# Kernel tuning notes

Measured on AMD Instinct MI355X. Metric: run time of the kernel, lower is better.

Reference implementation:

```python
import jax, jax.numpy as jnp
import numpy as np

B, N, E, DIN, H1, H2, DOUT = 2, 20000, 320000, 128, 256, 256, 128


def setup_inputs() -> dict:
    key = jax.random.key(0)
    ks = jax.random.split(key, 9)
    X = jax.random.normal(ks[0], (B, N, DIN), dtype=jnp.float32)
    edge_index = jax.random.randint(ks[1], (2, E), 0, N, dtype=jnp.int32)
    def lin(k, fan_in, fan_out):
        lim = 1.0 / np.sqrt(fan_in)
        return jax.random.uniform(k, (fan_in, fan_out), jnp.float32, -lim, lim)
    W1 = lin(ks[2], DIN, H1); b1 = jnp.zeros((H1,), jnp.float32)
    W2 = lin(ks[3], H1, H2);  b2 = jnp.zeros((H2,), jnp.float32)
    W3 = lin(ks[4], H2, DOUT); b3 = jnp.zeros((DOUT,), jnp.float32)
    prelu_a = jnp.array(0.25, jnp.float32)  # PReLU default single shared param
    return dict(X=X, W1=W1, b1=b1, W2=W2, b2=b2, W3=W3, b3=b3,
                prelu_a=prelu_a, edge_index=edge_index)


def reference(X, W1, b1, W2, b2, W3, b3, prelu_a, edge_index):
    src, dst = edge_index[0], edge_index[1]
    n = X.shape[1]
    # GCN symmetric normalization with self-loops: deg = in-degree + 1
    deg = jax.ops.segment_sum(jnp.ones_like(src, X.dtype), dst, num_segments=n) + 1.0
    dinv = jax.lax.rsqrt(deg)                      # [N]
    norm_e = dinv[src] * dinv[dst]                 # [E] edge norm
    norm_self = dinv * dinv                        # [N] self-loop norm

    def gcn(x, W, b):
        h = x @ W                                  # [N, F_out]
        agg = jax.ops.segment_sum(h[src] * norm_e[:, None], dst, num_segments=n)
        agg = agg + h * norm_self[:, None]         # add self-loop message
        return agg + b

    def prelu(x):
        return jnp.where(x >= 0, x, prelu_a * x)

    def single(x):  # x: [N, DIN]
        x = prelu(gcn(x, W1, b1))
        x = prelu(gcn(x, W2, b2))
        return gcn(x, W3, b3)

    return jax.vmap(single)(X)                     # [B, N, DOUT]
```

## Files before the change

kernel.cpp:

```cpp
#include <hip/hip_runtime.h>

#define NB 20000
#define EB 320000
#define DIN 128
#define H1D 256
#define H2D 256
#define DOUTD 128
#define SCAN_BLOCKS ((NB + 255) / 256)


__global__ void zero_kernel(int* __restrict__ p, int n) {
    int t = blockIdx.x * blockDim.x + threadIdx.x;
    if (t < n) p[t] = 0;
}

__global__ void hist_kernel(const int* __restrict__ dst, int* __restrict__ bins) {
    int t = blockIdx.x * blockDim.x + threadIdx.x;
    if (t < EB) atomicAdd(&bins[dst[t]], 1);
}

__global__ __launch_bounds__(256) void scanA_kernel(const int* __restrict__ bins,
                                                    int* __restrict__ loc,
                                                    int* __restrict__ blksum) {
    __shared__ int s[256];
    int t = threadIdx.x;
    int i = blockIdx.x * 256 + t;
    int v = (i < NB) ? bins[i] : 0;
    s[t] = v;
    __syncthreads();
    for (int off = 1; off < 256; off <<= 1) {
        int u = (t >= off) ? s[t - off] : 0;
        __syncthreads();
        s[t] += u;
        __syncthreads();
    }
    if (i < NB) loc[i] = s[t] - v;
    if (t == 255) blksum[blockIdx.x] = s[255];
}

__global__ __launch_bounds__(128) void scanB_kernel(int* __restrict__ blksum) {
    __shared__ int s[128];
    int t = threadIdx.x;
    int v = (t < SCAN_BLOCKS) ? blksum[t] : 0;
    s[t] = v;
    __syncthreads();
    for (int off = 1; off < 128; off <<= 1) {
        int u = (t >= off) ? s[t - off] : 0;
        __syncthreads();
        s[t] += u;
        __syncthreads();
    }
    if (t < SCAN_BLOCKS) blksum[t] = s[t] - v;
}

__global__ __launch_bounds__(256) void scanC_kernel(const int* __restrict__ bins,
                                                    const int* __restrict__ loc,
                                                    const int* __restrict__ blksum,
                                                    int* __restrict__ rs,
                                                    int* __restrict__ cursor,
                                                    float* __restrict__ dinv) {
    int i = blockIdx.x * 256 + threadIdx.x;
    if (i < NB) {
        int r = loc[i] + blksum[blockIdx.x];
        rs[i] = r;
        cursor[i] = r;
        dinv[i] = rsqrtf((float)bins[i] + 1.0f);
    }
    if (i == 0) rs[NB] = EB;
}

__global__ void scatter_kernel(const int* __restrict__ src, const int* __restrict__ dst,
                               const float* __restrict__ dinv,
                               int* __restrict__ cursor, int2* __restrict__ edges) {
    int t = blockIdx.x * blockDim.x + threadIdx.x;
    if (t < EB) {
        int d = dst[t], s = src[t];
        int p = atomicAdd(&cursor[d], 1);
        edges[p] = make_int2(s, __float_as_int(dinv[s] * dinv[d]));
    }
}


template <int NC>
__device__ inline void ldrow(float4 (&d)[NC], const float* __restrict__ p) {
#pragma unroll
    for (int c = 0; c < NC; ++c) d[c] = ((const float4*)p)[c];
}
template <int NC>
__device__ inline void fmarow(float4 (&a)[NC], const float4 (&t)[NC], float w) {
#pragma unroll
    for (int c = 0; c < NC; ++c) {
        a[c].x = fmaf(t[c].x, w, a[c].x);
        a[c].y = fmaf(t[c].y, w, a[c].y);
        a[c].z = fmaf(t[c].z, w, a[c].z);
        a[c].w = fmaf(t[c].w, w, a[c].w);
    }
}

template <int F, bool SPLIT_IN, bool SPLIT_OUT, bool BIAS, bool PRELU>
__global__ __launch_bounds__(256) void agg_kernel(
    const float* __restrict__ h, float* __restrict__ out,
    const int* __restrict__ rs, const int2* __restrict__ edges,
    const float* __restrict__ dinv, const float* __restrict__ bias,
    const float* __restrict__ pa) {
    constexpr int V2 = 2 * F / 64;
    constexpr int NC = V2 / 4;
    constexpr int GSTRIDE = SPLIT_IN ? F : 2 * F;
    int node = blockIdx.x * 4 + (threadIdx.x >> 6);
    int lane = threadIdx.x & 63;
    int b = lane >> 5;
    int fl = (lane & 31) * V2;

    const float* gbase = SPLIT_IN ? (h + (size_t)b * NB * F + fl)
                                  : (h + (size_t)lane * V2);

    float4 acc0[NC], acc1[NC], acc2[NC], acc3[NC];
    {
        float dv = dinv[node];
        float sw = dv * dv;
        float4 tv[NC];
        ldrow<NC>(tv, gbase + (size_t)node * GSTRIDE);
#pragma unroll
        for (int c = 0; c < NC; ++c) {
            acc0[c] = make_float4(tv[c].x * sw, tv[c].y * sw, tv[c].z * sw, tv[c].w * sw);
            acc1[c] = make_float4(0.f, 0.f, 0.f, 0.f);
            acc2[c] = make_float4(0.f, 0.f, 0.f, 0.f);
            acc3[c] = make_float4(0.f, 0.f, 0.f, 0.f);
        }
    }

    int e0 = __builtin_amdgcn_readfirstlane(rs[node]);
    int e1 = __builtin_amdgcn_readfirstlane(rs[node + 1]);
    int e = e0;
    for (; e + 4 <= e1; e += 4) {
        int2 d0 = edges[e], d1 = edges[e + 1], d2 = edges[e + 2], d3 = edges[e + 3];
        float4 t0[NC], t1[NC], t2[NC], t3[NC];
        ldrow<NC>(t0, gbase + (size_t)d0.x * GSTRIDE);
        ldrow<NC>(t1, gbase + (size_t)d1.x * GSTRIDE);
        ldrow<NC>(t2, gbase + (size_t)d2.x * GSTRIDE);
        ldrow<NC>(t3, gbase + (size_t)d3.x * GSTRIDE);
        fmarow<NC>(acc0, t0, __int_as_float(d0.y));
        fmarow<NC>(acc1, t1, __int_as_float(d1.y));
        fmarow<NC>(acc2, t2, __int_as_float(d2.y));
        fmarow<NC>(acc3, t3, __int_as_float(d3.y));
    }
    for (; e < e1; ++e) {
        int2 d0 = edges[e];
        float4 t0[NC];
        ldrow<NC>(t0, gbase + (size_t)d0.x * GSTRIDE);
        fmarow<NC>(acc0, t0, __int_as_float(d0.y));
    }

#pragma unroll
    for (int c = 0; c < NC; ++c) {
        acc0[c].x += (acc1[c].x + acc2[c].x) + acc3[c].x;
        acc0[c].y += (acc1[c].y + acc2[c].y) + acc3[c].y;
        acc0[c].z += (acc1[c].z + acc2[c].z) + acc3[c].z;
        acc0[c].w += (acc1[c].w + acc2[c].w) + acc3[c].w;
    }
    if (BIAS) {
        float4 bv[NC];
        ldrow<NC>(bv, bias + fl);
#pragma unroll
        for (int c = 0; c < NC; ++c) {
            acc0[c].x += bv[c].x; acc0[c].y += bv[c].y;
            acc0[c].z += bv[c].z; acc0[c].w += bv[c].w;
        }
    }
    if (PRELU) {
        float a = *pa;
#pragma unroll
        for (int c = 0; c < NC; ++c) {
            acc0[c].x = acc0[c].x >= 0.f ? acc0[c].x : a * acc0[c].x;
            acc0[c].y = acc0[c].y >= 0.f ? acc0[c].y : a * acc0[c].y;
            acc0[c].z = acc0[c].z >= 0.f ? acc0[c].z : a * acc0[c].z;
            acc0[c].w = acc0[c].w >= 0.f ? acc0[c].w : a * acc0[c].w;
        }
    }
    float* obase = SPLIT_OUT ? (out + (size_t)b * NB * F + (size_t)node * F + fl)
                             : (out + (size_t)node * 2 * F + lane * V2);
#pragma unroll
    for (int c = 0; c < NC; ++c) ((float4*)obase)[c] = acc0[c];
}

template <bool BIAS, bool PRELU>
__global__ __launch_bounds__(256) void gemm_kernel(const float* __restrict__ A, int M, int K,
                                                   const float* __restrict__ W, int Nc,
                                                   const float* __restrict__ bias,
                                                   const float* __restrict__ pa,
                                                   float* __restrict__ C) {
    __shared__ alignas(16) float As[16][132];
    __shared__ alignas(16) float Bs[16][68];
    int t = threadIdx.x;
    int bm = blockIdx.x * 128;
    int bn = blockIdx.y * 64;
    int tx = t & 15, ty = t >> 4;
    int m0 = ty * 8, n0 = tx * 4;
    int ar = t >> 2, ac4 = (t & 3) * 4;
    int br = t >> 4, bc4 = (t & 15) * 4;

    float acc[8][4] = {};

    for (int k0 = 0; k0 < K; k0 += 16) {
        float4 a0 = make_float4(0.f, 0.f, 0.f, 0.f), a1 = a0;
        int r0 = bm + ar, r1 = bm + ar + 64;
        if (r0 < M) a0 = *(const float4*)&A[(size_t)r0 * K + k0 + ac4];
        if (r1 < M) a1 = *(const float4*)&A[(size_t)r1 * K + k0 + ac4];
        As[ac4 + 0][ar] = a0.x; As[ac4 + 1][ar] = a0.y;
        As[ac4 + 2][ar] = a0.z; As[ac4 + 3][ar] = a0.w;
        As[ac4 + 0][ar + 64] = a1.x; As[ac4 + 1][ar + 64] = a1.y;
        As[ac4 + 2][ar + 64] = a1.z; As[ac4 + 3][ar + 64] = a1.w;
        float4 bv = *(const float4*)&W[(size_t)(k0 + br) * Nc + bn + bc4];
        *(float4*)&Bs[br][bc4] = bv;
        __syncthreads();
#pragma unroll
        for (int k = 0; k < 16; ++k) {
            float4 av0 = *(const float4*)&As[k][m0];
            float4 av1 = *(const float4*)&As[k][m0 + 4];
            float4 bv4 = *(const float4*)&Bs[k][n0];
            float a_[8] = {av0.x, av0.y, av0.z, av0.w, av1.x, av1.y, av1.z, av1.w};
            float b_[4] = {bv4.x, bv4.y, bv4.z, bv4.w};
#pragma unroll
            for (int i = 0; i < 8; ++i)
#pragma unroll
                for (int j = 0; j < 4; ++j)
                    acc[i][j] = fmaf(a_[i], b_[j], acc[i][j]);
        }
        __syncthreads();
    }

    float pav = 0.0f;
    if (PRELU) pav = *pa;
#pragma unroll
    for (int i = 0; i < 8; ++i) {
        int row = bm + m0 + i;
        if (row < M) {
            float v[4];
#pragma unroll
            for (int j = 0; j < 4; ++j) {
                float x = acc[i][j];
                if (BIAS) x += bias[bn + n0 + j];
                if (PRELU) x = (x >= 0.0f) ? x : pav * x;
                v[j] = x;
            }
            *(float4*)&C[(size_t)row * Nc + bn + n0] = make_float4(v[0], v[1], v[2], v[3]);
        }
    }
}


static inline char* carve(char*& p, size_t bytes) {
    char* r = p;
    p += (bytes + 255) & ~(size_t)255;
    return r;
}

extern "C" void kernel_launch(void* const* d_in, const int* in_sizes, int n_in,
                              void* d_out, int out_size, void* d_ws, size_t ws_size,
                              hipStream_t stream) {
    const float* X  = (const float*)d_in[0];
    const float* W1 = (const float*)d_in[1];
    const float* b1 = (const float*)d_in[2];
    const float* W2 = (const float*)d_in[3];
    const float* b2 = (const float*)d_in[4];
    const float* W3 = (const float*)d_in[5];
    const float* b3 = (const float*)d_in[6];
    const float* pa = (const float*)d_in[7];
    const int* ei   = (const int*)d_in[8];
    const int* src = ei;
    const int* dst = ei + EB;
    float* out = (float*)d_out;

    char* p = (char*)d_ws;
    int* bins    = (int*)carve(p, NB * sizeof(int));
    int* loc     = (int*)carve(p, NB * sizeof(int));
    int* blksum  = (int*)carve(p, 128 * sizeof(int));
    int* rs      = (int*)carve(p, (NB + 1) * sizeof(int));
    int* cursor  = (int*)carve(p, NB * sizeof(int));
    int2* edges  = (int2*)carve(p, EB * sizeof(int2));
    float* dinv  = (float*)carve(p, NB * sizeof(float));
    float* bufA  = (float*)carve(p, (size_t)2 * NB * 256 * sizeof(float));
    float* bufB  = (float*)carve(p, (size_t)2 * NB * 256 * sizeof(float));

    const int M = 2 * NB;

    zero_kernel<<<SCAN_BLOCKS, 256, 0, stream>>>(bins, NB);
    hist_kernel<<<(EB + 255) / 256, 256, 0, stream>>>(dst, bins);
    scanA_kernel<<<SCAN_BLOCKS, 256, 0, stream>>>(bins, loc, blksum);
    scanB_kernel<<<1, 128, 0, stream>>>(blksum);
    scanC_kernel<<<SCAN_BLOCKS, 256, 0, stream>>>(bins, loc, blksum, rs, cursor, dinv);
    scatter_kernel<<<(EB + 255) / 256, 256, 0, stream>>>(src, dst, dinv, cursor, edges);

    const int aggGrid = NB / 4;

    agg_kernel<128, true, false, false, false><<<aggGrid, 256, 0, stream>>>(
        X, bufA, rs, edges, dinv, nullptr, nullptr);
    gemm_kernel<true, true><<<dim3((M + 127) / 128, H1D / 64), 256, 0, stream>>>(
        bufA, M, DIN, W1, H1D, b1, pa, bufB);

    gemm_kernel<false, false><<<dim3((M + 127) / 128, H2D / 64), 256, 0, stream>>>(
        bufB, M, H1D, W2, H2D, nullptr, nullptr, bufA);
    agg_kernel<256, false, false, true, true><<<aggGrid, 256, 0, stream>>>(
        bufA, bufB, rs, edges, dinv, b2, pa);

    gemm_kernel<false, false><<<dim3((M + 127) / 128, DOUTD / 64), 256, 0, stream>>>(
        bufB, M, H2D, W3, DOUTD, nullptr, nullptr, bufA);
    agg_kernel<128, false, true, true, false><<<aggGrid, 256, 0, stream>>>(
        bufA, out, rs, edges, dinv, b3, nullptr);
}
```

Measured before the change: 394.9 us.

## Slice aggregation features into eight column slabs so gathers stay cache-resident

Replaces the one-node-per-wavefront aggregation kernel with a sliced version. Each block handles one of eight feature slices for a chunk of 160 nodes, and several nodes share a wavefront with a few lanes each. Restricting each block to an F/8 column slab shrinks the working set of the random neighbour gathers, which should raise L2/MALL hit rates. Edge records are read with nontemporal loads. In exchange, the edge list and row pointers are re-read eight times, each lane holds fewer accumulators and gets less memory-level parallelism per edge, and lanes diverge because neighbouring nodes in a wave have different degrees.

```diff
diff --git a/kernel.cpp b/kernel.cpp
--- a/kernel.cpp
+++ b/kernel.cpp
@@ -7,6 +7,7 @@
 #define H2D 256
 #define DOUTD 128
 #define SCAN_BLOCKS ((NB + 255) / 256)
+#define NPB 160
 
 
 __global__ void zero_kernel(int* __restrict__ p, int n) {
@@ -81,106 +82,83 @@
 }
 
 
-template <int NC>
-__device__ inline void ldrow(float4 (&d)[NC], const float* __restrict__ p) {
-#pragma unroll
-    for (int c = 0; c < NC; ++c) d[c] = ((const float4*)p)[c];
-}
-template <int NC>
-__device__ inline void fmarow(float4 (&a)[NC], const float4 (&t)[NC], float w) {
-#pragma unroll
-    for (int c = 0; c < NC; ++c) {
-        a[c].x = fmaf(t[c].x, w, a[c].x);
-        a[c].y = fmaf(t[c].y, w, a[c].y);
-        a[c].z = fmaf(t[c].z, w, a[c].z);
-        a[c].w = fmaf(t[c].w, w, a[c].w);
-    }
-}
-
 template <int F, bool SPLIT_IN, bool SPLIT_OUT, bool BIAS, bool PRELU>
-__global__ __launch_bounds__(256) void agg_kernel(
+__global__ __launch_bounds__(256) void aggs_kernel(
     const float* __restrict__ h, float* __restrict__ out,
     const int* __restrict__ rs, const int2* __restrict__ edges,
     const float* __restrict__ dinv, const float* __restrict__ bias,
     const float* __restrict__ pa) {
-    constexpr int V2 = 2 * F / 64;
-    constexpr int NC = V2 / 4;
+    constexpr int SLW = F / 8;
+    constexpr int LPB = SLW / 4;
+    constexpr int LPE = 2 * LPB;
+    constexpr int NG = 64 / LPE;
+    constexpr int STEP = 4 * NG;
+    constexpr int ITER = NPB / STEP;
     constexpr int GSTRIDE = SPLIT_IN ? F : 2 * F;
-    int node = blockIdx.x * 4 + (threadIdx.x >> 6);
-    int lane = threadIdx.x & 63;
-    int b = lane >> 5;
-    int fl = (lane & 31) * V2;
-
-    const float* gbase = SPLIT_IN ? (h + (size_t)b * NB * F + fl)
-                                  : (h + (size_t)lane * V2);
-
-    float4 acc0[NC], acc1[NC], acc2[NC], acc3[NC];
-    {
-        float dv = dinv[node];
+    constexpr int OSTRIDE = SPLIT_OUT ? F : 2 * F;
+
+    const int s = blockIdx.x & 7;
+    const int chunk = blockIdx.x >> 3;
+    const int wid = threadIdx.x >> 6;
+    const int lane = threadIdx.x & 63;
+    const int g = lane / LPE;
+    const int li = lane % LPE;
+    const int b = li / LPB;
+    const int c = li % LPB;
+    const int foff = s * SLW + c * 4;
+
+    const float* gbase = h + (SPLIT_IN ? (size_t)b * NB * F : (size_t)b * F) + foff;
+    float* obase = out + (SPLIT_OUT ? (size_t)b * NB * F : (size_t)b * F) + foff;
+
+    const float pav = PRELU ? *pa : 0.0f;
+    float4 bv = make_float4(0.f, 0.f, 0.f, 0.f);
+    if (BIAS) bv = *(const float4*)(bias + foff);
+
+    int n = chunk * NPB + wid * NG + g;
+#pragma unroll 1
+    for (int i = 0; i < ITER; ++i, n += STEP) {
+        int e0 = rs[n], e1 = rs[n + 1];
+        float4 a0 = make_float4(0.f, 0.f, 0.f, 0.f);
+        float4 a1 = make_float4(0.f, 0.f, 0.f, 0.f);
+        int e = e0;
+        for (; e + 2 <= e1; e += 2) {
+            long long r0 = __builtin_nontemporal_load((const long long*)(edges + e));
+            long long r1 = __builtin_nontemporal_load((const long long*)(edges + e + 1));
+            int s0 = (int)r0, s1 = (int)r1;
+            float w0 = __int_as_float((int)(r0 >> 32));
+            float w1 = __int_as_float((int)(r1 >> 32));
+            float4 t0 = *(const float4*)(gbase + (size_t)s0 * GSTRIDE);
+            float4 t1 = *(const float4*)(gbase + (size_t)s1 * GSTRIDE);
+            a0.x = fmaf(t0.x, w0, a0.x); a0.y = fmaf(t0.y, w0, a0.y);
+            a0.z = fmaf(t0.z, w0, a0.z); a0.w = fmaf(t0.w, w0, a0.w);
+            a1.x = fmaf(t1.x, w1, a1.x); a1.y = fmaf(t1.y, w1, a1.y);
+            a1.z = fmaf(t1.z, w1, a1.z); a1.w = fmaf(t1.w, w1, a1.w);
+        }
+        if (e < e1) {
+            long long r0 = __builtin_nontemporal_load((const long long*)(edges + e));
+            int s0 = (int)r0;
+            float w0 = __int_as_float((int)(r0 >> 32));
+            float4 t0 = *(const float4*)(gbase + (size_t)s0 * GSTRIDE);
+            a0.x = fmaf(t0.x, w0, a0.x); a0.y = fmaf(t0.y, w0, a0.y);
+            a0.z = fmaf(t0.z, w0, a0.z); a0.w = fmaf(t0.w, w0, a0.w);
+        }
+        float dv = dinv[n];
         float sw = dv * dv;
-        float4 tv[NC];
-        ldrow<NC>(tv, gbase + (size_t)node * GSTRIDE);
-#pragma unroll
-        for (int c = 0; c < NC; ++c) {
-            acc0[c] = make_float4(tv[c].x * sw, tv[c].y * sw, tv[c].z * sw, tv[c].w * sw);
-            acc1[c] = make_float4(0.f, 0.f, 0.f, 0.f);
-            acc2[c] = make_float4(0.f, 0.f, 0.f, 0.f);
-            acc3[c] = make_float4(0.f, 0.f, 0.f, 0.f);
-        }
-    }
-
-    int e0 = __builtin_amdgcn_readfirstlane(rs[node]);
-    int e1 = __builtin_amdgcn_readfirstlane(rs[node + 1]);
-    int e = e0;
-    for (; e + 4 <= e1; e += 4) {
-        int2 d0 = edges[e], d1 = edges[e + 1], d2 = edges[e + 2], d3 = edges[e + 3];
-        float4 t0[NC], t1[NC], t2[NC], t3[NC];
-        ldrow<NC>(t0, gbase + (size_t)d0.x * GSTRIDE);
-        ldrow<NC>(t1, gbase + (size_t)d1.x * GSTRIDE);
-        ldrow<NC>(t2, gbase + (size_t)d2.x * GSTRIDE);
-        ldrow<NC>(t3, gbase + (size_t)d3.x * GSTRIDE);
-        fmarow<NC>(acc0, t0, __int_as_float(d0.y));
-        fmarow<NC>(acc1, t1, __int_as_float(d1.y));
-        fmarow<NC>(acc2, t2, __int_as_float(d2.y));
-        fmarow<NC>(acc3, t3, __int_as_float(d3.y));
-    }
-    for (; e < e1; ++e) {
-        int2 d0 = edges[e];
-        float4 t0[NC];
-        ldrow<NC>(t0, gbase + (size_t)d0.x * GSTRIDE);
-        fmarow<NC>(acc0, t0, __int_as_float(d0.y));
-    }
-
-#pragma unroll
-    for (int c = 0; c < NC; ++c) {
-        acc0[c].x += (acc1[c].x + acc2[c].x) + acc3[c].x;
-        acc0[c].y += (acc1[c].y + acc2[c].y) + acc3[c].y;
-        acc0[c].z += (acc1[c].z + acc2[c].z) + acc3[c].z;
-        acc0[c].w += (acc1[c].w + acc2[c].w) + acc3[c].w;
-    }
-    if (BIAS) {
-        float4 bv[NC];
-        ldrow<NC>(bv, bias + fl);
-#pragma unroll
-        for (int c = 0; c < NC; ++c) {
-            acc0[c].x += bv[c].x; acc0[c].y += bv[c].y;
-            acc0[c].z += bv[c].z; acc0[c].w += bv[c].w;
-        }
-    }
-    if (PRELU) {
-        float a = *pa;
-#pragma unroll
-        for (int c = 0; c < NC; ++c) {
-            acc0[c].x = acc0[c].x >= 0.f ? acc0[c].x : a * acc0[c].x;
-            acc0[c].y = acc0[c].y >= 0.f ? acc0[c].y : a * acc0[c].y;
-            acc0[c].z = acc0[c].z >= 0.f ? acc0[c].z : a * acc0[c].z;
-            acc0[c].w = acc0[c].w >= 0.f ? acc0[c].w : a * acc0[c].w;
-        }
-    }
-    float* obase = SPLIT_OUT ? (out + (size_t)b * NB * F + (size_t)node * F + fl)
-                             : (out + (size_t)node * 2 * F + lane * V2);
-#pragma unroll
-    for (int c = 0; c < NC; ++c) ((float4*)obase)[c] = acc0[c];
+        float4 ts = *(const float4*)(gbase + (size_t)n * GSTRIDE);
+        float4 r;
+        r.x = fmaf(ts.x, sw, a0.x + a1.x);
+        r.y = fmaf(ts.y, sw, a0.y + a1.y);
+        r.z = fmaf(ts.z, sw, a0.z + a1.z);
+        r.w = fmaf(ts.w, sw, a0.w + a1.w);
+        if (BIAS) { r.x += bv.x; r.y += bv.y; r.z += bv.z; r.w += bv.w; }
+        if (PRELU) {
+            r.x = r.x >= 0.f ? r.x : pav * r.x;
+            r.y = r.y >= 0.f ? r.y : pav * r.y;
+            r.z = r.z >= 0.f ? r.z : pav * r.z;
+            r.w = r.w >= 0.f ? r.w : pav * r.w;
+        }
+        *(float4*)(obase + (size_t)n * OSTRIDE) = r;
+    }
 }
 
 template <bool BIAS, bool PRELU>
@@ -291,20 +269,20 @@
     scanC_kernel<<<SCAN_BLOCKS, 256, 0, stream>>>(bins, loc, blksum, rs, cursor, dinv);
     scatter_kernel<<<(EB + 255) / 256, 256, 0, stream>>>(src, dst, dinv, cursor, edges);
 
-    const int aggGrid = NB / 4;
-
-    agg_kernel<128, true, false, false, false><<<aggGrid, 256, 0, stream>>>(
+    const int aggGrid = (NB / NPB) * 8;
+
+    aggs_kernel<128, true, false, false, false><<<aggGrid, 256, 0, stream>>>(
         X, bufA, rs, edges, dinv, nullptr, nullptr);
     gemm_kernel<true, true><<<dim3((M + 127) / 128, H1D / 64), 256, 0, stream>>>(
         bufA, M, DIN, W1, H1D, b1, pa, bufB);
 
     gemm_kernel<false, false><<<dim3((M + 127) / 128, H2D / 64), 256, 0, stream>>>(
         bufB, M, H1D, W2, H2D, nullptr, nullptr, bufA);
-    agg_kernel<256, false, false, true, true><<<aggGrid, 256, 0, stream>>>(
+    aggs_kernel<256, false, false, true, true><<<aggGrid, 256, 0, stream>>>(
         bufA, bufB, rs, edges, dinv, b2, pa);
 
     gemm_kernel<false, false><<<dim3((M + 127) / 128, DOUTD / 64), 256, 0, stream>>>(
         bufB, M, H2D, W3, DOUTD, nullptr, nullptr, bufA);
-    agg_kernel<128, false, true, true, false><<<aggGrid, 256, 0, stream>>>(
+    aggs_kernel<128, false, true, true, false><<<aggGrid, 256, 0, stream>>>(
         bufA, out, rs, edges, dinv, b3, nullptr);
 }
```

Result: slower. 542.2 us (+37.3%).

## Split batch and co-schedule GEMM and aggregation blocks in fused launches

Applied to the files above, without the earlier changes.

Drops the interleaved two-batch aggregation layout and processes each batch element separately. The other batch's GEMM and aggregation now share a launch, with blocks split between GEMM tiles and aggregation nodes. Memory-bound gathers can then overlap compute-bound GEMM tiles and fill the GPU better. The cost is one-wave-per-node aggregation with narrower per-lane vectors and more launches overall. The shared __shared__ arrays inside the device bodies also change occupancy for the aggregation blocks.

```diff
diff --git a/kernel.cpp b/kernel.cpp
--- a/kernel.cpp
+++ b/kernel.cpp
@@ -81,119 +81,94 @@
 }
 
 
-template <int NC>
-__device__ inline void ldrow(float4 (&d)[NC], const float* __restrict__ p) {
-#pragma unroll
-    for (int c = 0; c < NC; ++c) d[c] = ((const float4*)p)[c];
-}
-template <int NC>
-__device__ inline void fmarow(float4 (&a)[NC], const float4 (&t)[NC], float w) {
-#pragma unroll
-    for (int c = 0; c < NC; ++c) {
-        a[c].x = fmaf(t[c].x, w, a[c].x);
-        a[c].y = fmaf(t[c].y, w, a[c].y);
-        a[c].z = fmaf(t[c].z, w, a[c].z);
-        a[c].w = fmaf(t[c].w, w, a[c].w);
-    }
-}
-
-template <int F, bool SPLIT_IN, bool SPLIT_OUT, bool BIAS, bool PRELU>
-__global__ __launch_bounds__(256) void agg_kernel(
-    const float* __restrict__ h, float* __restrict__ out,
-    const int* __restrict__ rs, const int2* __restrict__ edges,
-    const float* __restrict__ dinv, const float* __restrict__ bias,
-    const float* __restrict__ pa) {
-    constexpr int V2 = 2 * F / 64;
-    constexpr int NC = V2 / 4;
-    constexpr int GSTRIDE = SPLIT_IN ? F : 2 * F;
-    int node = blockIdx.x * 4 + (threadIdx.x >> 6);
+__device__ inline void vload(float (&d)[4], const float* p) {
+    float4 t = *(const float4*)p; d[0] = t.x; d[1] = t.y; d[2] = t.z; d[3] = t.w;
+}
+__device__ inline void vload(float (&d)[2], const float* p) {
+    float2 t = *(const float2*)p; d[0] = t.x; d[1] = t.y;
+}
+__device__ inline void vstore(float* p, const float (&d)[4]) {
+    *(float4*)p = make_float4(d[0], d[1], d[2], d[3]);
+}
+__device__ inline void vstore(float* p, const float (&d)[2]) {
+    *(float2*)p = make_float2(d[0], d[1]);
+}
+
+template <int F, bool BIAS, bool PRELU>
+__device__ void agg_body(int ablk,
+                         const float* __restrict__ h, float* __restrict__ out,
+                         const int* __restrict__ rs, const int2* __restrict__ edges,
+                         const float* __restrict__ dinv, const float* __restrict__ bias,
+                         const float* __restrict__ pa) {
+    constexpr int VEC = F / 64;
+    int wid = threadIdx.x >> 6;
     int lane = threadIdx.x & 63;
-    int b = lane >> 5;
-    int fl = (lane & 31) * V2;
-
-    const float* gbase = SPLIT_IN ? (h + (size_t)b * NB * F + fl)
-                                  : (h + (size_t)lane * V2);
-
-    float4 acc0[NC], acc1[NC], acc2[NC], acc3[NC];
+    int node = ablk * 4 + wid;
+    const float* hsrc = h + (size_t)lane * VEC;
+
+    float acc0[VEC], acc1[VEC] = {}, acc2[VEC] = {}, acc3[VEC] = {};
     {
         float dv = dinv[node];
         float sw = dv * dv;
-        float4 tv[NC];
-        ldrow<NC>(tv, gbase + (size_t)node * GSTRIDE);
-#pragma unroll
-        for (int c = 0; c < NC; ++c) {
-            acc0[c] = make_float4(tv[c].x * sw, tv[c].y * sw, tv[c].z * sw, tv[c].w * sw);
-            acc1[c] = make_float4(0.f, 0.f, 0.f, 0.f);
-            acc2[c] = make_float4(0.f, 0.f, 0.f, 0.f);
-            acc3[c] = make_float4(0.f, 0.f, 0.f, 0.f);
-        }
-    }
-
+        float t[VEC];
+        vload(t, hsrc + (size_t)node * F);
+#pragma unroll
+        for (int v = 0; v < VEC; ++v) acc0[v] = t[v] * sw;
+    }
     int e0 = __builtin_amdgcn_readfirstlane(rs[node]);
     int e1 = __builtin_amdgcn_readfirstlane(rs[node + 1]);
     int e = e0;
     for (; e + 4 <= e1; e += 4) {
         int2 d0 = edges[e], d1 = edges[e + 1], d2 = edges[e + 2], d3 = edges[e + 3];
-        float4 t0[NC], t1[NC], t2[NC], t3[NC];
-        ldrow<NC>(t0, gbase + (size_t)d0.x * GSTRIDE);
-        ldrow<NC>(t1, gbase + (size_t)d1.x * GSTRIDE);
-        ldrow<NC>(t2, gbase + (size_t)d2.x * GSTRIDE);
-        ldrow<NC>(t3, gbase + (size_t)d3.x * GSTRIDE);
-        fmarow<NC>(acc0, t0, __int_as_float(d0.y));
-        fmarow<NC>(acc1, t1, __int_as_float(d1.y));
-        fmarow<NC>(acc2, t2, __int_as_float(d2.y));
-        fmarow<NC>(acc3, t3, __int_as_float(d3.y));
+        float t0[VEC], t1[VEC], t2[VEC], t3[VEC];
+        vload(t0, hsrc + (size_t)d0.x * F);
+        vload(t1, hsrc + (size_t)d1.x * F);
+        vload(t2, hsrc + (size_t)d2.x * F);
+        vload(t3, hsrc + (size_t)d3.x * F);
+        float w0 = __int_as_float(d0.y), w1 = __int_as_float(d1.y);
+        float w2 = __int_as_float(d2.y), w3 = __int_as_float(d3.y);
+#pragma unroll
+        for (int v = 0; v < VEC; ++v) {
+            acc0[v] = fmaf(t0[v], w0, acc0[v]);
+            acc1[v] = fmaf(t1[v], w1, acc1[v]);
+            acc2[v] = fmaf(t2[v], w2, acc2[v]);
+            acc3[v] = fmaf(t3[v], w3, acc3[v]);
+        }
     }
     for (; e < e1; ++e) {
         int2 d0 = edges[e];
-        float4 t0[NC];
-        ldrow<NC>(t0, gbase + (size_t)d0.x * GSTRIDE);
-        fmarow<NC>(acc0, t0, __int_as_float(d0.y));
-    }
-
-#pragma unroll
-    for (int c = 0; c < NC; ++c) {
-        acc0[c].x += (acc1[c].x + acc2[c].x) + acc3[c].x;
-        acc0[c].y += (acc1[c].y + acc2[c].y) + acc3[c].y;
-        acc0[c].z += (acc1[c].z + acc2[c].z) + acc3[c].z;
-        acc0[c].w += (acc1[c].w + acc2[c].w) + acc3[c].w;
-    }
+        float t0[VEC];
+        vload(t0, hsrc + (size_t)d0.x * F);
+        float w0 = __int_as_float(d0.y);
+#pragma unroll
+        for (int v = 0; v < VEC; ++v) acc0[v] = fmaf(t0[v], w0, acc0[v]);
+    }
+#pragma unroll
+    for (int v = 0; v < VEC; ++v) acc0[v] += (acc1[v] + acc2[v]) + acc3[v];
     if (BIAS) {
-        float4 bv[NC];
-        ldrow<NC>(bv, bias + fl);
-#pragma unroll
-        for (int c = 0; c < NC; ++c) {
-            acc0[c].x += bv[c].x; acc0[c].y += bv[c].y;
-            acc0[c].z += bv[c].z; acc0[c].w += bv[c].w;
-        }
+        float bv[VEC];
+        vload(bv, bias + lane * VEC);
+#pragma unroll
+        for (int v = 0; v < VEC; ++v) acc0[v] += bv[v];
     }
     if (PRELU) {
         float a = *pa;
 #pragma unroll
-        for (int c = 0; c < NC; ++c) {
-            acc0[c].x = acc0[c].x >= 0.f ? acc0[c].x : a * acc0[c].x;
-            acc0[c].y = acc0[c].y >= 0.f ? acc0[c].y : a * acc0[c].y;
-            acc0[c].z = acc0[c].z >= 0.f ? acc0[c].z : a * acc0[c].z;
-            acc0[c].w = acc0[c].w >= 0.f ? acc0[c].w : a * acc0[c].w;
-        }
-    }
-    float* obase = SPLIT_OUT ? (out + (size_t)b * NB * F + (size_t)node * F + fl)
-                             : (out + (size_t)node * 2 * F + lane * V2);
-#pragma unroll
-    for (int c = 0; c < NC; ++c) ((float4*)obase)[c] = acc0[c];
+        for (int v = 0; v < VEC; ++v) acc0[v] = acc0[v] >= 0.0f ? acc0[v] : a * acc0[v];
+    }
+    vstore(out + (size_t)node * F + lane * VEC, acc0);
 }
 
 template <bool BIAS, bool PRELU>
-__global__ __launch_bounds__(256) void gemm_kernel(const float* __restrict__ A, int M, int K,
-                                                   const float* __restrict__ W, int Nc,
-                                                   const float* __restrict__ bias,
-                                                   const float* __restrict__ pa,
-                                                   float* __restrict__ C) {
+__device__ void gemm_body(int gx, const float* __restrict__ A, int M, int K,
+                          const float* __restrict__ W, int Nc,
+                          const float* __restrict__ bias, const float* __restrict__ pa,
+                          float* __restrict__ C, int mt) {
     __shared__ alignas(16) float As[16][132];
     __shared__ alignas(16) float Bs[16][68];
     int t = threadIdx.x;
-    int bm = blockIdx.x * 128;
-    int bn = blockIdx.y * 64;
+    int bm = (gx % mt) * 128;
+    int bn = (gx / mt) * 64;
     int tx = t & 15, ty = t >> 4;
     int m0 = ty * 8, n0 = tx * 4;
     int ar = t >> 2, ac4 = (t & 3) * 4;
@@ -245,6 +220,42 @@
             }
             *(float4*)&C[(size_t)row * Nc + bn + n0] = make_float4(v[0], v[1], v[2], v[3]);
         }
+    }
+}
+
+
+template <int F, bool BIAS, bool PRELU>
+__global__ __launch_bounds__(256) void agg_kernel(
+    const float* __restrict__ h, float* __restrict__ out,
+    const int* __restrict__ rs, const int2* __restrict__ edges,
+    const float* __restrict__ dinv, const float* __restrict__ bias,
+    const float* __restrict__ pa) {
+    agg_body<F, BIAS, PRELU>(blockIdx.x, h, out, rs, edges, dinv, bias, pa);
+}
+
+template <bool BIAS, bool PRELU>
+__global__ __launch_bounds__(256) void gemm_kernel(
+    const float* __restrict__ A, int M, int K, const float* __restrict__ W, int Nc,
+    const float* __restrict__ bias, const float* __restrict__ pa,
+    float* __restrict__ C, int mt) {
+    gemm_body<BIAS, PRELU>(blockIdx.x, A, M, K, W, Nc, bias, pa, C, mt);
+}
+
+template <int AF, bool AB, bool AP, bool GB, bool GP>
+__global__ __launch_bounds__(256) void fat_kernel(
+    const float* __restrict__ A, int M, int K, const float* __restrict__ W, int Nc,
+    const float* __restrict__ gbias, float* __restrict__ C, int mt, int ng,
+    const float* __restrict__ ah, float* __restrict__ aout,
+    const int* __restrict__ rs, const int2* __restrict__ edges,
+    const float* __restrict__ dinv, const float* __restrict__ abias,
+    const float* __restrict__ pa, int total) {
+    int bx = blockIdx.x;
+    int p0 = (int)((long long)bx * ng / total);
+    int p1 = (int)(((long long)bx + 1) * ng / total);
+    if (p1 > p0) {
+        gemm_body<GB, GP>(p0, A, M, K, W, Nc, gbias, pa, C, mt);
+    } else {
+        agg_body<AF, AB, AP>(bx - p1, ah, aout, rs, edges, dinv, abias, pa);
     }
 }
 
@@ -279,10 +290,15 @@
     int* cursor  = (int*)carve(p, NB * sizeof(int));
     int2* edges  = (int2*)carve(p, EB * sizeof(int2));
     float* dinv  = (float*)carve(p, NB * sizeof(float));
-    float* bufA  = (float*)carve(p, (size_t)2 * NB * 256 * sizeof(float));
-    float* bufB  = (float*)carve(p, (size_t)2 * NB * 256 * sizeof(float));
-
-    const int M = 2 * NB;
+    float* P0 = (float*)carve(p, (size_t)NB * 256 * sizeof(float));
+    float* Q0 = (float*)carve(p, (size_t)NB * 256 * sizeof(float));
+    float* P1 = (float*)carve(p, (size_t)NB * 256 * sizeof(float));
+    float* Q1 = (float*)carve(p, (size_t)NB * 256 * sizeof(float));
+
+    const float* X0 = X;
+    const float* X1 = X + (size_t)NB * DIN;
+    float* out0 = out;
+    float* out1 = out + (size_t)NB * DOUTD;
 
     zero_kernel<<<SCAN_BLOCKS, 256, 0, stream>>>(bins, NB);
     hist_kernel<<<(EB + 255) / 256, 256, 0, stream>>>(dst, bins);
@@ -291,20 +307,36 @@
     scanC_kernel<<<SCAN_BLOCKS, 256, 0, stream>>>(bins, loc, blksum, rs, cursor, dinv);
     scatter_kernel<<<(EB + 255) / 256, 256, 0, stream>>>(src, dst, dinv, cursor, edges);
 
-    const int aggGrid = NB / 4;
-
-    agg_kernel<128, true, false, false, false><<<aggGrid, 256, 0, stream>>>(
-        X, bufA, rs, edges, dinv, nullptr, nullptr);
-    gemm_kernel<true, true><<<dim3((M + 127) / 128, H1D / 64), 256, 0, stream>>>(
-        bufA, M, DIN, W1, H1D, b1, pa, bufB);
-
-    gemm_kernel<false, false><<<dim3((M + 127) / 128, H2D / 64), 256, 0, stream>>>(
-        bufB, M, H1D, W2, H2D, nullptr, nullptr, bufA);
-    agg_kernel<256, false, false, true, true><<<aggGrid, 256, 0, stream>>>(
-        bufA, bufB, rs, edges, dinv, b2, pa);
-
-    gemm_kernel<false, false><<<dim3((M + 127) / 128, DOUTD / 64), 256, 0, stream>>>(
-        bufB, M, H2D, W3, DOUTD, nullptr, nullptr, bufA);
-    agg_kernel<128, false, true, true, false><<<aggGrid, 256, 0, stream>>>(
-        bufA, out, rs, edges, dinv, b3, nullptr);
-}
+    const int AGG_BLK = NB / 4;
+    const int MT = (NB + 127) / 128;
+    const int NG_256 = MT * (256 / 64);
+    const int NG_128 = MT * (128 / 64);
+
+
+    agg_kernel<128, false, false><<<AGG_BLK, 256, 0, stream>>>(
+        X0, P0, rs, edges, dinv, nullptr, nullptr);
+
+    fat_kernel<128, false, false, true, true><<<NG_256 + AGG_BLK, 256, 0, stream>>>(
+        P0, NB, DIN, W1, H1D, b1, Q0, MT, NG_256,
+        X1, P1, rs, edges, dinv, nullptr, pa, NG_256 + AGG_BLK);
+
+    gemm_kernel<false, false><<<NG_256, 256, 0, stream>>>(
+        Q0, NB, H1D, W2, H2D, nullptr, nullptr, P0, MT);
+    gemm_kernel<true, true><<<NG_256, 256, 0, stream>>>(
+        P1, NB, DIN, W1, H1D, b1, pa, Q1, MT);
+
+    fat_kernel<256, true, true, false, false><<<NG_256 + AGG_BLK, 256, 0, stream>>>(
+        Q1, NB, H1D, W2, H2D, nullptr, P1, MT, NG_256,
+        P0, Q0, rs, edges, dinv, b2, pa, NG_256 + AGG_BLK);
+
+    fat_kernel<256, true, true, false, false><<<NG_128 + AGG_BLK, 256, 0, stream>>>(
+        Q0, NB, H2D, W3, DOUTD, nullptr, P0, MT, NG_128,
+        P1, Q1, rs, edges, dinv, b2, pa, NG_128 + AGG_BLK);
+
+    fat_kernel<128, true, false, false, false><<<NG_128 + AGG_BLK, 256, 0, stream>>>(
+        Q1, NB, H2D, W3, DOUTD, nullptr, P1, MT, NG_128,
+        P0, out0, rs, edges, dinv, b3, nullptr, NG_128 + AGG_BLK);
+
+    agg_kernel<128, true, false><<<AGG_BLK, 256, 0, stream>>>(
+        P1, out1, rs, edges, dinv, b3, nullptr);
+}
```

Result: slower. 444.9 us (+12.7%).
